# Kernel tuning notes

Measured on AMD Instinct MI355X. Metric: run time of the kernel, lower is better.

The kernel has to match this reference:

```python
import jax, jax.numpy as jnp
import numpy as np

N_NODES = 100000


def gcn_layer(x, W, b, src, dst, norm, n):
    # x: [N, Fin] -> linear transform then normalized scatter-add aggregation
    h = x @ W                                   # [N, Fout]
    msgs = h[src] * norm[:, None]               # [E+N, Fout] edge messages
    out = jax.ops.segment_sum(msgs, dst, num_segments=n)
    return out + b


def _build_graph(edge_index, n):
    # add self loops (PyG GCNConv default)
    loops = jnp.arange(n, dtype=edge_index.dtype)
    src = jnp.concatenate([edge_index[0], loops])
    dst = jnp.concatenate([edge_index[1], loops])
    deg = jax.ops.segment_sum(jnp.ones_like(dst, dtype=jnp.float32), dst, num_segments=n)
    dis = jnp.where(deg > 0, jax.lax.rsqrt(deg), 0.0)  # deg^{-1/2}
    norm = dis[src] * dis[dst]                  # symmetric normalization per edge
    return src, dst, norm


def setup_inputs() -> dict:
    key = jax.random.key(0)
    ks = jax.random.split(key, 8)
    x = jax.random.normal(ks[0], (N_NODES, 3), dtype=jnp.float32)
    edge_index = jax.random.randint(ks[1], (2, 6400000), 0, N_NODES, dtype=jnp.int32)
    def glorot(k, fin, fout):
        s = jnp.sqrt(6.0 / (fin + fout))
        return jax.random.uniform(k, (fin, fout), jnp.float32, -s, s)
    return {
        "x": x,
        "edge_index": edge_index,
        "W1": glorot(ks[2], 3, 32), "b1": jnp.zeros((32,), jnp.float32),
        "W2": glorot(ks[3], 32, 32), "b2": jnp.zeros((32,), jnp.float32),
        "W3": glorot(ks[4], 32, 1), "b3": jnp.zeros((1,), jnp.float32),
    }


def reference(x, edge_index, W1, b1, W2, b2, W3, b3):
    n = x.shape[0]
    src, dst, norm = _build_graph(edge_index, n)
    h = jax.nn.relu(gcn_layer(x, W1, b1, src, dst, norm, n))
    h = jax.nn.relu(gcn_layer(h, W2, b2, src, dst, norm, n))
    return gcn_layer(h, W3, b3, src, dst, norm, n)
```

## Files before the change

kernel.cpp:

```cpp
#include <hip/hip_runtime.h>
#include <hip/hip_fp16.h>


#define BLK 256
#define BLK2 512
#define SB 1000
#define CHUNK 6400
#define BKT 128
#define NBKT 782
#define MAXNB 1024
#define BUFSZ 9400

__global__ void k_hist(const int* __restrict__ dst, int* __restrict__ hist, int E) {
    __shared__ int lh[2][NBKT];
    for (int b = threadIdx.x; b < 2 * NBKT; b += blockDim.x)
        ((int*)lh)[b] = 0;
    __syncthreads();
    int t = threadIdx.x;
    int sub = (t >> 8) & 1;
    int beg = blockIdx.x * CHUNK;
    int end = min(E, beg + CHUNK);
    int nq = (end - beg) >> 2;
    const int4* d4 = (const int4*)(dst + beg);
    for (int i = t; i < nq; i += blockDim.x) {
        int4 d = d4[i];
        atomicAdd(&lh[sub][d.x >> 7], 1);
        atomicAdd(&lh[sub][d.y >> 7], 1);
        atomicAdd(&lh[sub][d.z >> 7], 1);
        atomicAdd(&lh[sub][d.w >> 7], 1);
    }
    for (int e = beg + (nq << 2) + t; e < end; e += blockDim.x)
        atomicAdd(&lh[sub][dst[e] >> 7], 1);
    __syncthreads();
    for (int b = t; b < NBKT; b += blockDim.x)
        hist[(size_t)blockIdx.x * NBKT + b] = lh[0][b] + lh[1][b];
}

__global__ void k_scanA(int* __restrict__ hist, int* __restrict__ btot, int NB) {
    int b = blockIdx.x, t = threadIdx.x;
    int base = t * 2;
    int v0 = (base + 0 < SB) ? hist[(size_t)(base + 0) * NB + b] : 0;
    int v1 = (base + 1 < SB) ? hist[(size_t)(base + 1) * NB + b] : 0;
    int s = v0 + v1;
    int lane = t & 63, w = t >> 6;
    int x = s;
#pragma unroll
    for (int off = 1; off < 64; off <<= 1) {
        int u = __shfl_up(x, off, 64);
        if (lane >= off) x += u;
    }
    __shared__ int wsum[8];
    if (lane == 63) wsum[w] = x;
    __syncthreads();
    int woff = 0;
    for (int k = 0; k < 8; k++) woff += (k < w) ? wsum[k] : 0;
    int run = woff + x - s;
    if (base + 0 < SB) hist[(size_t)(base + 0) * NB + b] = run;  run += v0;
    if (base + 1 < SB) hist[(size_t)(base + 1) * NB + b] = run;  run += v1;
    if (t == 511) btot[b] = run;
}

__global__ void k_scanB(const int* __restrict__ btot, int* __restrict__ bbase,
                        int NB, int E) {
    __shared__ int sh[MAXNB];
    int t = threadIdx.x;
    int v = (t < NB) ? btot[t] : 0;
    sh[t] = v;
    __syncthreads();
    for (int off = 1; off < MAXNB; off <<= 1) {
        int u = (t >= off) ? sh[t - off] : 0;
        __syncthreads();
        sh[t] += u;
        __syncthreads();
    }
    if (t < NB) bbase[t] = sh[t] - v;
    if (t == 0) bbase[NB] = E;
}

__global__ void k_bsort(const int* __restrict__ src, const int* __restrict__ dst,
                        const int* __restrict__ hist, const int* __restrict__ btot,
                        const int* __restrict__ bbase,
                        unsigned int* __restrict__ packed, int E) {
    __shared__ unsigned int bufB[CHUNK];
    __shared__ unsigned short binarr2[CHUNK];
    __shared__ int cnt[NBKT];
    __shared__ int off[NBKT];
    __shared__ int cur[NBKT];
    __shared__ int gbase[NBKT];
    __shared__ int wsum[8];
    int t = threadIdx.x;
    int beg = blockIdx.x * CHUNK;
    int end = min(E, beg + CHUNK);
    int len = end - beg;
    int last = (blockIdx.x + 1 == gridDim.x);
    for (int b = t; b < NBKT; b += blockDim.x) {
        int my = hist[(size_t)blockIdx.x * NBKT + b];
        int nx = last ? btot[b] : hist[(size_t)(blockIdx.x + 1) * NBKT + b];
        cnt[b] = nx - my;
        gbase[b] = bbase[b] + my;
    }
    __syncthreads();
    {
        int base = t * 2;
        int v0 = (base + 0 < NBKT) ? cnt[base + 0] : 0;
        int v1 = (base + 1 < NBKT) ? cnt[base + 1] : 0;
        int s = v0 + v1;
        int lane = t & 63, w = t >> 6;
        int x = s;
#pragma unroll
        for (int o = 1; o < 64; o <<= 1) {
            int u = __shfl_up(x, o, 64);
            if (lane >= o) x += u;
        }
        if (lane == 63) wsum[w] = x;
        __syncthreads();
        int woff = 0;
        for (int k = 0; k < 8; k++) woff += (k < w) ? wsum[k] : 0;
        int run = woff + x - s;
        if (base + 0 < NBKT) { off[base + 0] = run; cur[base + 0] = run; } run += v0;
        if (base + 1 < NBKT) { off[base + 1] = run; cur[base + 1] = run; } run += v1;
    }
    __syncthreads();
    for (int i = t; i < len; i += blockDim.x) {
        int d = dst[beg + i];
        int s = src[beg + i];
        int b = d >> 7;
        int pos = atomicAdd(&cur[b], 1);
        bufB[pos] = (unsigned)s | ((unsigned)(d & 127) << 17);
        binarr2[pos] = (unsigned short)b;
    }
    __syncthreads();
    for (int i = t; i < len; i += blockDim.x) {
        int b = binarr2[i];
        packed[gbase[b] + i - off[b]] = bufB[i];
    }
}

__global__ void k_sort(unsigned int* __restrict__ packed, const int* __restrict__ bbase,
                       const float* __restrict__ x, float* __restrict__ dis,
                       uint2* __restrict__ y8, int* __restrict__ rowptr, int N, int E) {
    __shared__ unsigned int buf[BUFSZ];
    __shared__ int cnt4[4][BKT];
    __shared__ int cur[BKT];
    __shared__ int wsum[2];
    int b = blockIdx.x, t = threadIdx.x;
    int beg = bbase[b], end = bbase[b + 1];
    int len = end - beg;
    for (int k = t; k < 4 * BKT; k += blockDim.x) ((int*)cnt4)[k] = 0;
    __syncthreads();
    int sub = (t >> 7) & 3;
    for (int i = t; i < len; i += blockDim.x) {
        unsigned v = packed[beg + i];
        buf[i] = v;
        atomicAdd(&cnt4[sub][v >> 17], 1);
    }
    __syncthreads();
    int v0 = 0, xs = 0;
    if (t < BKT) {
        v0 = cnt4[0][t] + cnt4[1][t] + cnt4[2][t] + cnt4[3][t];
        xs = v0;
#pragma unroll
        for (int o = 1; o < 64; o <<= 1) {
            int u = __shfl_up(xs, o, 64);
            if ((t & 63) >= o) xs += u;
        }
        if ((t & 63) == 63) wsum[t >> 6] = xs;
    }
    __syncthreads();
    if (t < BKT) {
        int woff = (t >= 64) ? wsum[0] : 0;
        int excl = woff + xs - v0;
        cur[t] = excl;
        int gi = b * BKT + t;
        if (gi < N) {
            rowptr[gi] = beg + excl;
            float di = rsqrtf((float)v0 + 1.0f);
            dis[gi] = di;
            uint2 yv;
            *(__half2*)&yv.x = __floats2half2_rn(di * x[3 * gi + 0],
                                                 di * x[3 * gi + 1]);
            *(__half2*)&yv.y = __floats2half2_rn(di * x[3 * gi + 2], 0.f);
            y8[gi] = yv;
        }
    }
    __syncthreads();
    for (int i = t; i < len; i += blockDim.x) {
        unsigned vv = buf[i];
        int pos = atomicAdd(&cur[vv >> 17], 1);
        packed[beg + pos] = vv & 0x1FFFF;
    }
    if (b == 0 && t == 0) rowptr[N] = E;
}

__global__ void k_l1(const unsigned int* __restrict__ csr, const int* __restrict__ rowptr,
                     const uint2* __restrict__ y8, const float* __restrict__ dis,
                     const float* __restrict__ W1, const float* __restrict__ b1,
                     __half* __restrict__ g, int N) {
    int t = blockIdx.x * blockDim.x + threadIdx.x;
    int i = t >> 5, j = t & 31;
    if (i >= N) return;
    int beg = rowptr[i], end = rowptr[i + 1];
    float ax = 0.f, ay = 0.f, az = 0.f;
    for (int e = beg + j; e < end; e += 32) {
        uint2 v = y8[csr[e]];
        float2 fa = __half22float2(*(const __half2*)&v.x);
        float2 fb = __half22float2(*(const __half2*)&v.y);
        ax += fa.x; ay += fa.y; az += fb.x;
    }
#pragma unroll
    for (int m = 16; m >= 1; m >>= 1) {
        ax += __shfl_xor(ax, m, 32);
        ay += __shfl_xor(ay, m, 32);
        az += __shfl_xor(az, m, 32);
    }
    float di = dis[i];
    uint2 vs = y8[i];
    float2 sa = __half22float2(*(const __half2*)&vs.x);
    float2 sb = __half22float2(*(const __half2*)&vs.y);
    float a0 = di * (ax + sa.x);
    float a1 = di * (ay + sa.y);
    float a2 = di * (az + sb.x);
    float h = b1[j] + a0 * W1[j] + a1 * W1[32 + j] + a2 * W1[64 + j];
    g[(size_t)i * 32 + j] = __float2half(di * fmaxf(h, 0.f));
}

__device__ __forceinline__ void acc4(float& c0, float& c1, float& c2, float& c3,
                                     uint2 r) {
    __half2 a = *(const __half2*)&r.x;
    __half2 b = *(const __half2*)&r.y;
    float2 fa = __half22float2(a);
    float2 fb = __half22float2(b);
    c0 += fa.x; c1 += fa.y; c2 += fb.x; c3 += fb.y;
}

__global__ void k_l2(const unsigned int* __restrict__ csr, const int* __restrict__ rowptr,
                     const __half* __restrict__ g, const float* __restrict__ dis,
                     const float* __restrict__ W2, const float* __restrict__ b2,
                     const float* __restrict__ W3, float* __restrict__ q, int N) {
    __shared__ float sW2[1024];
    __shared__ float sb2[32];
    __shared__ float sW3[32];
    int tid = threadIdx.x;
    ((float4*)sW2)[tid] = ((const float4*)W2)[tid];
    if (tid < 32) { sb2[tid] = b2[tid]; sW3[tid] = W3[tid]; }
    __syncthreads();
    int t = blockIdx.x * blockDim.x + tid;
    int i = t >> 3, j = t & 7;
    if (i >= N) return;
    int beg = rowptr[i], end = rowptr[i + 1];
    const uint2* g2 = (const uint2*)g;
    float pa0 = 0.f, pa1 = 0.f, pa2 = 0.f, pa3 = 0.f;
    float pb0 = 0.f, pb1 = 0.f, pb2 = 0.f, pb3 = 0.f;
    float pc0 = 0.f, pc1 = 0.f, pc2 = 0.f, pc3 = 0.f;
    float pd0 = 0.f, pd1 = 0.f, pd2 = 0.f, pd3 = 0.f;
    int e = beg;
    for (; e < end && (e & 3); e++) {
        int s = (int)csr[e];
        uint2 r = g2[s * 8 + j];
        acc4(pa0, pa1, pa2, pa3, r);
    }
    for (; e + 16 <= end; e += 16) {
        int4 ca = *(const int4*)(csr + e);
        int4 cb = *(const int4*)(csr + e + 4);
        int4 cc = *(const int4*)(csr + e + 8);
        int4 cd = *(const int4*)(csr + e + 12);
        uint2 r0  = g2[ca.x * 8 + j];
        uint2 r1  = g2[ca.y * 8 + j];
        uint2 r2  = g2[ca.z * 8 + j];
        uint2 r3  = g2[ca.w * 8 + j];
        uint2 r4  = g2[cb.x * 8 + j];
        uint2 r5  = g2[cb.y * 8 + j];
        uint2 r6  = g2[cb.z * 8 + j];
        uint2 r7  = g2[cb.w * 8 + j];
        uint2 r8  = g2[cc.x * 8 + j];
        uint2 r9  = g2[cc.y * 8 + j];
        uint2 r10 = g2[cc.z * 8 + j];
        uint2 r11 = g2[cc.w * 8 + j];
        uint2 r12 = g2[cd.x * 8 + j];
        uint2 r13 = g2[cd.y * 8 + j];
        uint2 r14 = g2[cd.z * 8 + j];
        uint2 r15 = g2[cd.w * 8 + j];
        acc4(pa0, pa1, pa2, pa3, r0);
        acc4(pb0, pb1, pb2, pb3, r1);
        acc4(pc0, pc1, pc2, pc3, r2);
        acc4(pd0, pd1, pd2, pd3, r3);
        acc4(pa0, pa1, pa2, pa3, r4);
        acc4(pb0, pb1, pb2, pb3, r5);
        acc4(pc0, pc1, pc2, pc3, r6);
        acc4(pd0, pd1, pd2, pd3, r7);
        acc4(pa0, pa1, pa2, pa3, r8);
        acc4(pb0, pb1, pb2, pb3, r9);
        acc4(pc0, pc1, pc2, pc3, r10);
        acc4(pd0, pd1, pd2, pd3, r11);
        acc4(pa0, pa1, pa2, pa3, r12);
        acc4(pb0, pb1, pb2, pb3, r13);
        acc4(pc0, pc1, pc2, pc3, r14);
        acc4(pd0, pd1, pd2, pd3, r15);
    }
    for (; e + 8 <= end; e += 8) {
        int4 ca = *(const int4*)(csr + e);
        int4 cb = *(const int4*)(csr + e + 4);
        uint2 r0 = g2[ca.x * 8 + j];
        uint2 r1 = g2[ca.y * 8 + j];
        uint2 r2 = g2[ca.z * 8 + j];
        uint2 r3 = g2[ca.w * 8 + j];
        uint2 r4 = g2[cb.x * 8 + j];
        uint2 r5 = g2[cb.y * 8 + j];
        uint2 r6 = g2[cb.z * 8 + j];
        uint2 r7 = g2[cb.w * 8 + j];
        acc4(pa0, pa1, pa2, pa3, r0);
        acc4(pb0, pb1, pb2, pb3, r1);
        acc4(pc0, pc1, pc2, pc3, r2);
        acc4(pd0, pd1, pd2, pd3, r3);
        acc4(pa0, pa1, pa2, pa3, r4);
        acc4(pb0, pb1, pb2, pb3, r5);
        acc4(pc0, pc1, pc2, pc3, r6);
        acc4(pd0, pd1, pd2, pd3, r7);
    }
    for (; e < end; e++) {
        int s = (int)csr[e];
        uint2 r = g2[s * 8 + j];
        acc4(pa0, pa1, pa2, pa3, r);
    }
    float c0 = (pa0 + pb0) + (pc0 + pd0);
    float c1 = (pa1 + pb1) + (pc1 + pd1);
    float c2 = (pa2 + pb2) + (pc2 + pd2);
    float c3 = (pa3 + pb3) + (pc3 + pd3);
    float di = dis[i];
    uint2 rs = g2[i * 8 + j];
    float2 sa = __half22float2(*(const __half2*)&rs.x);
    float2 sb = __half22float2(*(const __half2*)&rs.y);
    float a0 = di * (c0 + sa.x);
    float a1 = di * (c1 + sa.y);
    float a2 = di * (c2 + sb.x);
    float a3 = di * (c3 + sb.y);
    int m = 4 * j;
    float4 bo = *(const float4*)&sb2[m];
    float o0 = bo.x, o1 = bo.y, o2 = bo.z, o3 = bo.w;
#pragma unroll
    for (int kl = 0; kl < 8; kl++) {
        float x0 = __shfl(a0, kl, 8);
        float x1 = __shfl(a1, kl, 8);
        float x2 = __shfl(a2, kl, 8);
        float x3 = __shfl(a3, kl, 8);
        float4 w0 = *(const float4*)&sW2[(4 * kl + 0) * 32 + m];
        float4 w1 = *(const float4*)&sW2[(4 * kl + 1) * 32 + m];
        float4 w2 = *(const float4*)&sW2[(4 * kl + 2) * 32 + m];
        float4 w3 = *(const float4*)&sW2[(4 * kl + 3) * 32 + m];
        o0 = fmaf(x0, w0.x, fmaf(x1, w1.x, fmaf(x2, w2.x, fmaf(x3, w3.x, o0))));
        o1 = fmaf(x0, w0.y, fmaf(x1, w1.y, fmaf(x2, w2.y, fmaf(x3, w3.y, o1))));
        o2 = fmaf(x0, w0.z, fmaf(x1, w1.z, fmaf(x2, w2.z, fmaf(x3, w3.z, o2))));
        o3 = fmaf(x0, w0.w, fmaf(x1, w1.w, fmaf(x2, w2.w, fmaf(x3, w3.w, o3))));
    }
    float4 wv = *(const float4*)&sW3[m];
    float cc = fmaxf(o0, 0.f) * wv.x + fmaxf(o1, 0.f) * wv.y
             + fmaxf(o2, 0.f) * wv.z + fmaxf(o3, 0.f) * wv.w;
    cc += __shfl_xor(cc, 1, 8);
    cc += __shfl_xor(cc, 2, 8);
    cc += __shfl_xor(cc, 4, 8);
    if (j == 0) q[i] = di * cc;
}

__global__ void k_l3(const unsigned int* __restrict__ csr, const int* __restrict__ rowptr,
                     const float* __restrict__ q, const float* __restrict__ dis,
                     const float* __restrict__ b3, float* __restrict__ out, int N) {
    int t = blockIdx.x * blockDim.x + threadIdx.x;
    int i = t >> 5, j = t & 31;
    if (i >= N) return;
    int beg = rowptr[i], end = rowptr[i + 1];
    float acc = 0.f;
    for (int e = beg + j; e < end; e += 32)
        acc += q[csr[e]];
#pragma unroll
    for (int m = 16; m >= 1; m >>= 1)
        acc += __shfl_xor(acc, m, 32);
    if (j == 0) out[i] = dis[i] * (acc + q[i]) + b3[0];
}

extern "C" void kernel_launch(void* const* d_in, const int* in_sizes, int n_in,
                              void* d_out, int out_size, void* d_ws, size_t ws_size,
                              hipStream_t stream) {
    const float* x  = (const float*)d_in[0];
    const int*   ei = (const int*)d_in[1];
    const float* W1 = (const float*)d_in[2];
    const float* b1 = (const float*)d_in[3];
    const float* W2 = (const float*)d_in[4];
    const float* b2 = (const float*)d_in[5];
    const float* W3 = (const float*)d_in[6];
    const float* b3 = (const float*)d_in[7];
    float* out = (float*)d_out;

    int N = in_sizes[0] / 3;
    int E = in_sizes[1] / 2;
    const int* src = ei;
    const int* dst = ei + E;

    char* w = (char*)d_ws;
#define CARVE(nbytes) w; w += (((size_t)(nbytes) + 255) & ~(size_t)255)
    int*   hist   = (int*)  CARVE((size_t)SB * NBKT * 4);
    int*   btot   = (int*)  CARVE((size_t)MAXNB * 4);
    int*   bbase  = (int*)  CARVE((size_t)(MAXNB + 1) * 4);
    int*   rowptr = (int*)  CARVE((size_t)(N + 1) * 4);
    float* dis    = (float*)CARVE((size_t)N * 4);
    uint2* y8     = (uint2*)CARVE((size_t)N * 8);
    __half* g     = (__half*)CARVE((size_t)N * 32 * 2);
    float* q      = (float*)CARVE((size_t)N * 4);
    unsigned int* packed = (unsigned int*)CARVE((size_t)E * 4);
#undef CARVE

    k_hist <<<SB, BLK2, 0, stream>>>(dst, hist, E);
    k_scanA<<<NBKT, BLK2, 0, stream>>>(hist, btot, NBKT);
    k_scanB<<<1, MAXNB, 0, stream>>>(btot, bbase, NBKT, E);
    k_bsort<<<SB, BLK2, 0, stream>>>(src, dst, hist, btot, bbase, packed, E);
    k_sort <<<NBKT, BLK2, 0, stream>>>(packed, bbase, x, dis, y8, rowptr, N, E);

    long long tn = (long long)N * 32;
    unsigned gn = (unsigned)((tn + BLK - 1) / BLK);
    long long tn8 = (long long)N * 8;
    unsigned gn8 = (unsigned)((tn8 + BLK - 1) / BLK);
    k_l1<<<gn,  BLK, 0, stream>>>(packed, rowptr, y8, dis, W1, b1, g, N);
    k_l2<<<gn8, BLK, 0, stream>>>(packed, rowptr, g, dis, W2, b2, W3, q, N);
    k_l3<<<gn,  BLK, 0, stream>>>(packed, rowptr, q, dis, b3, out, N);
}
```

Baseline: 316.5 us.

## Shrink bucket-sort chunk size and streamline per-block offset setup

The edge chunk per block drops from 6400 to 5120, so more blocks (1250) run the histogram and bucket-sort passes, and the cross-block scan is widened to three entries per thread to cover them. In k_bsort, the count/offset computation is done in registers, removing the separate shared cnt/off/gbase arrays and one barrier. The write-out now uses a single precomputed gdelta per bucket instead of gbase and off. The smaller shared-memory footprint may allow more resident blocks per CU, at the cost of more histogram rows to scan and shorter per-bucket runs in each chunk.

```diff
diff --git a/kernel.cpp b/kernel.cpp
--- a/kernel.cpp
+++ b/kernel.cpp
@@ -4,8 +4,8 @@
 
 #define BLK 256
 #define BLK2 512
-#define SB 1000
-#define CHUNK 6400
+#define SB 1250
+#define CHUNK 5120
 #define BKT 128
 #define NBKT 782
 #define MAXNB 1024
@@ -38,10 +38,11 @@
 
 __global__ void k_scanA(int* __restrict__ hist, int* __restrict__ btot, int NB) {
     int b = blockIdx.x, t = threadIdx.x;
-    int base = t * 2;
+    int base = t * 3;
     int v0 = (base + 0 < SB) ? hist[(size_t)(base + 0) * NB + b] : 0;
     int v1 = (base + 1 < SB) ? hist[(size_t)(base + 1) * NB + b] : 0;
-    int s = v0 + v1;
+    int v2 = (base + 2 < SB) ? hist[(size_t)(base + 2) * NB + b] : 0;
+    int s = v0 + v1 + v2;
     int lane = t & 63, w = t >> 6;
     int x = s;
 #pragma unroll
@@ -57,6 +58,7 @@
     int run = woff + x - s;
     if (base + 0 < SB) hist[(size_t)(base + 0) * NB + b] = run;  run += v0;
     if (base + 1 < SB) hist[(size_t)(base + 1) * NB + b] = run;  run += v1;
+    if (base + 2 < SB) hist[(size_t)(base + 2) * NB + b] = run;  run += v2;
     if (t == 511) btot[b] = run;
 }
 
@@ -83,57 +85,55 @@
                         unsigned int* __restrict__ packed, int E) {
     __shared__ unsigned int bufB[CHUNK];
     __shared__ unsigned short binarr2[CHUNK];
-    __shared__ int cnt[NBKT];
-    __shared__ int off[NBKT];
     __shared__ int cur[NBKT];
-    __shared__ int gbase[NBKT];
+    __shared__ int gdelta[NBKT];
     __shared__ int wsum[8];
     int t = threadIdx.x;
     int beg = blockIdx.x * CHUNK;
     int end = min(E, beg + CHUNK);
     int len = end - beg;
     int last = (blockIdx.x + 1 == gridDim.x);
-    for (int b = t; b < NBKT; b += blockDim.x) {
-        int my = hist[(size_t)blockIdx.x * NBKT + b];
-        int nx = last ? btot[b] : hist[(size_t)(blockIdx.x + 1) * NBKT + b];
-        cnt[b] = nx - my;
-        gbase[b] = bbase[b] + my;
-    }
-    __syncthreads();
-    {
-        int base = t * 2;
-        int v0 = (base + 0 < NBKT) ? cnt[base + 0] : 0;
-        int v1 = (base + 1 < NBKT) ? cnt[base + 1] : 0;
-        int s = v0 + v1;
-        int lane = t & 63, w = t >> 6;
-        int x = s;
-#pragma unroll
-        for (int o = 1; o < 64; o <<= 1) {
-            int u = __shfl_up(x, o, 64);
-            if (lane >= o) x += u;
-        }
-        if (lane == 63) wsum[w] = x;
-        __syncthreads();
-        int woff = 0;
-        for (int k = 0; k < 8; k++) woff += (k < w) ? wsum[k] : 0;
-        int run = woff + x - s;
-        if (base + 0 < NBKT) { off[base + 0] = run; cur[base + 0] = run; } run += v0;
-        if (base + 1 < NBKT) { off[base + 1] = run; cur[base + 1] = run; } run += v1;
-    }
+    int b0 = 2 * t, b1 = 2 * t + 1;
+    int c0 = 0, c1 = 0, gb0 = 0, gb1 = 0;
+    if (b0 < NBKT) {
+        int my = hist[(size_t)blockIdx.x * NBKT + b0];
+        int nx = last ? btot[b0] : hist[(size_t)(blockIdx.x + 1) * NBKT + b0];
+        c0 = nx - my;
+        gb0 = bbase[b0] + my;
+    }
+    if (b1 < NBKT) {
+        int my = hist[(size_t)blockIdx.x * NBKT + b1];
+        int nx = last ? btot[b1] : hist[(size_t)(blockIdx.x + 1) * NBKT + b1];
+        c1 = nx - my;
+        gb1 = bbase[b1] + my;
+    }
+    int s = c0 + c1;
+    int lane = t & 63, w = t >> 6;
+    int x = s;
+#pragma unroll
+    for (int o = 1; o < 64; o <<= 1) {
+        int u = __shfl_up(x, o, 64);
+        if (lane >= o) x += u;
+    }
+    if (lane == 63) wsum[w] = x;
+    __syncthreads();
+    int woff = 0;
+    for (int k = 0; k < 8; k++) woff += (k < w) ? wsum[k] : 0;
+    int run = woff + x - s;
+    if (b0 < NBKT) { cur[b0] = run; gdelta[b0] = gb0 - run; } run += c0;
+    if (b1 < NBKT) { cur[b1] = run; gdelta[b1] = gb1 - run; }
     __syncthreads();
     for (int i = t; i < len; i += blockDim.x) {
         int d = dst[beg + i];
-        int s = src[beg + i];
+        int sid = src[beg + i];
         int b = d >> 7;
         int pos = atomicAdd(&cur[b], 1);
-        bufB[pos] = (unsigned)s | ((unsigned)(d & 127) << 17);
+        bufB[pos] = (unsigned)sid | ((unsigned)(d & 127) << 17);
         binarr2[pos] = (unsigned short)b;
     }
     __syncthreads();
-    for (int i = t; i < len; i += blockDim.x) {
-        int b = binarr2[i];
-        packed[gbase[b] + i - off[b]] = bufB[i];
-    }
+    for (int i = t; i < len; i += blockDim.x)
+        packed[gdelta[binarr2[i]] + i] = bufB[i];
 }
 
 __global__ void k_sort(unsigned int* __restrict__ packed, const int* __restrict__ bbase,
```

Result: no change. 319.9 us (+1.1%).
